# Kernel optimization log

Measured on AMD Instinct MI355X. Metric: run time of the kernel, lower is better.

## Reference

```python
import jax, jax.numpy as jnp
import numpy as np

B, P, T = 128, 196, 20
VOCAB, ENC, EMB, DEC, ATTN = 10000, 2048, 512, 512, 512


def _linear_params(key, out_dim, in_dim):
    kw, kb = jax.random.split(key)
    s = 1.0 / np.sqrt(in_dim)
    W = jax.random.uniform(kw, (out_dim, in_dim), minval=-s, maxval=s, dtype=jnp.float32)
    b = jax.random.uniform(kb, (out_dim,), minval=-s, maxval=s, dtype=jnp.float32)
    return W, b


def setup_inputs() -> dict:
    key = jax.random.key(0)
    ks = jax.random.split(key, 12)
    enc_w, enc_b = _linear_params(ks[0], ATTN, ENC)
    dec_w, dec_b = _linear_params(ks[1], ATTN, DEC)
    full_w, full_b = _linear_params(ks[2], 1, ATTN)
    W_ih, b_ih = _linear_params(ks[3], 4 * DEC, EMB + ENC)
    W_hh, b_hh = _linear_params(ks[4], 4 * DEC, DEC)
    ih_w, ih_b = _linear_params(ks[5], DEC, ENC)
    ic_w, ic_b = _linear_params(ks[6], DEC, ENC)
    fc_w, fc_b = _linear_params(ks[7], VOCAB, DEC)
    return {
        "encoder_out": jax.random.normal(ks[8], (B, P, ENC), dtype=jnp.float32),
        "captions": jax.random.randint(ks[9], (B, T), 0, VOCAB, dtype=jnp.int32),
        "lengths": jax.random.randint(ks[10], (B,), 1, T + 1, dtype=jnp.int32),
        "embedding": jax.random.normal(ks[11], (VOCAB, EMB), dtype=jnp.float32),
        "enc_attn_w": enc_w, "enc_attn_b": enc_b,
        "dec_attn_w": dec_w, "dec_attn_b": dec_b,
        "full_attn_w": full_w, "full_attn_b": full_b,
        "W_ih": W_ih, "b_ih": b_ih, "W_hh": W_hh, "b_hh": b_hh,
        "init_h_w": ih_w, "init_h_b": ih_b,
        "init_c_w": ic_w, "init_c_b": ic_b,
        "fc_w": fc_w, "fc_b": fc_b,
    }


def reference(encoder_out, captions, lengths, embedding,
              enc_attn_w, enc_attn_b, dec_attn_w, dec_attn_b,
              full_attn_w, full_attn_b, W_ih, b_ih, W_hh, b_hh,
              init_h_w, init_h_b, init_c_w, init_c_b, fc_w, fc_b):
    # init hidden state from mean-pooled encoder features
    mean_enc = encoder_out.mean(axis=1)                      # [B, ENC]
    h = mean_enc @ init_h_w.T + init_h_b                      # [B, DEC]
    c = mean_enc @ init_c_w.T + init_c_b

    # loop-invariant encoder projection for additive attention
    attn_enc = jnp.einsum('bpe,ae->bpa', encoder_out, enc_attn_w) + enc_attn_b  # [B, P, ATTN]

    embs = embedding[captions]                                # [B, T, EMB]
    embs_t = jnp.swapaxes(embs, 0, 1)                         # [T, B, EMB]

    dec = h.shape[1]

    def step(carry, emb_t):
        h, c = carry
        # additive attention
        attn_dec = h @ dec_attn_w.T + dec_attn_b              # [B, ATTN]
        energy = jnp.einsum('bpa,a->bp', jax.nn.relu(attn_enc + attn_dec[:, None, :]), full_attn_w[0]) + full_attn_b[0]
        alpha = jax.nn.softmax(energy, axis=1)                # [B, P]
        context = jnp.einsum('bpe,bp->be', encoder_out, alpha)  # [B, ENC]
        # LSTMCell
        x = jnp.concatenate([emb_t, context], axis=1)
        gates = x @ W_ih.T + b_ih + h @ W_hh.T + b_hh          # [B, 4*DEC]
        i, f, g, o = jnp.split(gates, 4, axis=1)
        c_new = jax.nn.sigmoid(f) * c + jax.nn.sigmoid(i) * jnp.tanh(g)
        h_new = jax.nn.sigmoid(o) * jnp.tanh(c_new)
        preds = h_new @ fc_w.T + fc_b                          # [B, VOCAB] (dropout in eval mode = identity)
        return (h_new, c_new), (preds, alpha)

    (_, _), (outputs_t, alphas_t) = jax.lax.scan(step, (h, c), embs_t)
    outputs = jnp.swapaxes(outputs_t, 0, 1)                   # [B, T, VOCAB]
    alphas = jnp.swapaxes(alphas_t, 0, 1)                     # [B, T, P]
    return outputs, alphas
```

## Files before the change

### kernel.cpp

```cpp
#include <hip/hip_runtime.h>

constexpr int kB = 128, kP = 196, kT = 20;
constexpr int kVocab = 10000, kEnc = 2048, kEmb = 512, kDec = 512, kAttn = 512;

typedef __bf16 b16x8 __attribute__((ext_vector_type(8)));
typedef __bf16 b16x4 __attribute__((ext_vector_type(4)));
typedef float f32x4 __attribute__((ext_vector_type(4)));
typedef unsigned short u16x4 __attribute__((ext_vector_type(4)));

__device__ __forceinline__ unsigned short f2bf(float f) {
  unsigned int u = __float_as_uint(f);
  u += 0x7fffu + ((u >> 16) & 1u);
  return (unsigned short)(u >> 16);
}
__device__ __forceinline__ float bf2f(unsigned short h) {
  return __uint_as_float(((unsigned int)h) << 16);
}

__device__ __forceinline__ void async16(const void* g, void* l) {
  __builtin_amdgcn_global_load_lds(
      (const __attribute__((address_space(1))) unsigned int*)g,
      (__attribute__((address_space(3))) unsigned int*)l, 16, 0, 0);
}

template <int MODE>
__global__ __launch_bounds__(256) void gemm128(
    const unsigned short* __restrict__ A, const unsigned short* __restrict__ W,
    const float* __restrict__ bias, unsigned short* __restrict__ Cb,
    float* __restrict__ Cf, int K, int Nv) {
  __shared__ unsigned short sA[2][128 * 64];
  __shared__ unsigned short sB[2][128 * 64];
  const int tid = threadIdx.x;
  const int lane = tid & 63, wave = tid >> 6;
  const int wm = wave >> 1, wn = wave & 1;
  const int q = lane >> 4, l = lane & 15;
  const int nwg = gridDim.x * gridDim.y;
  const int orig = blockIdx.y * gridDim.x + blockIdx.x;
  const int qc = nwg >> 3, rc = nwg & 7;
  const int xcd = orig & 7, o8 = orig >> 3;
  const int wg = (xcd < rc ? xcd * (qc + 1) : rc * (qc + 1) + (xcd - rc) * qc) + o8;
  const int m0 = (wg / gridDim.x) * 128, n0 = (wg % gridDim.x) * 128;
  const int row0 = tid & 127, ch0 = tid >> 7;
  const long arow = (long)(m0 + row0) * K;
  const long brow = (long)(n0 + row0) * K;
  f32x4 acc[4][4] = {};

  auto stage = [&](int buf, int k0) {
#pragma unroll
    for (int cc = 0; cc < 4; cc++) {
      const int ch = ch0 + cc * 2;
      async16(A + arow + k0 + ch * 8, &sA[buf][(ch * 128 + row0) * 8]);
      async16(W + brow + k0 + ch * 8, &sB[buf][(ch * 128 + row0) * 8]);
    }
  };

  stage(0, 0);
  __syncthreads();
  int cur = 0;
  for (int k0 = 0; k0 < K; k0 += 64) {
    const bool last = (k0 + 64 >= K);
    if (!last) stage(cur ^ 1, k0 + 64);
    b16x8 af[2][4], bfr[2][4];
#pragma unroll
    for (int u = 0; u < 2; u++) {
      const int cb = u * 4 + q;
#pragma unroll
      for (int i = 0; i < 4; i++)
        af[u][i] = *(const b16x8*)&sA[cur][(cb * 128 + wm * 64 + 16 * i + l) * 8];
#pragma unroll
      for (int j = 0; j < 4; j++)
        bfr[u][j] = *(const b16x8*)&sB[cur][(cb * 128 + wn * 64 + 16 * j + l) * 8];
    }
#pragma unroll
    for (int u = 0; u < 2; u++)
#pragma unroll
      for (int i = 0; i < 4; i++)
#pragma unroll
        for (int j = 0; j < 4; j++)
          acc[i][j] = __builtin_amdgcn_mfma_f32_16x16x32_bf16(af[u][i], bfr[u][j], acc[i][j], 0, 0, 0);
    if (!last) {
      __syncthreads();
      cur ^= 1;
    }
  }

#pragma unroll
  for (int i = 0; i < 4; i++) {
    const int row = m0 + wm * 64 + 16 * i + q * 4;
#pragma unroll
    for (int j = 0; j < 4; j++) {
      const int col = n0 + wn * 64 + 16 * j + l;
      if (col >= Nv) continue;
      const float bv = bias[col];
#pragma unroll
      for (int r = 0; r < 4; r++) {
        const float v = acc[i][j][r] + bv;
        if (MODE == 0) {
          Cb[(long)(row + r) * kAttn + col] = f2bf(v);
        } else {
          const int rr = row + r;
          Cf[((long)(rr & 127) * kT + (rr >> 7)) * (long)kVocab + col] = v;
        }
      }
    }
  }
}

template <bool A_BF16, bool OUT_BF16>
__global__ __launch_bounds__(256) void gemm_bt(
    const void* __restrict__ A_, const unsigned short* __restrict__ W,
    const float* __restrict__ bias, float* __restrict__ C,
    unsigned short* __restrict__ Cb, int M, int N, int K, long ldc) {
  const int lane = threadIdx.x & 63;
  const int wave = threadIdx.x >> 6;
  const int wm = wave >> 1, wn = wave & 1;
  const int m0 = blockIdx.y * 64 + wm * 32;
  const int n0 = blockIdx.x * 64 + wn * 32;
  const int q = lane >> 4;
  const int l = lane & 15;
  f32x4 acc[2][2] = {};
  const unsigned short* Ab = (const unsigned short*)A_;
  const float* Af = (const float*)A_;

  for (int k0 = 0; k0 < K; k0 += 32) {
    const int ka = k0 + q * 8;
    b16x8 af[2], wf[2];
#pragma unroll
    for (int i = 0; i < 2; i++) {
      int r = m0 + 16 * i + l;
      if (r >= M) r = M - 1;
      if (A_BF16) {
        af[i] = *(const b16x8*)(Ab + (long)r * K + ka);
      } else {
        const float* p = Af + (long)r * K + ka;
        const f32x4 lo = *(const f32x4*)p;
        const f32x4 hi = *(const f32x4*)(p + 4);
        b16x8 t;
#pragma unroll
        for (int j = 0; j < 4; j++) {
          ((unsigned short*)&t)[j] = f2bf(lo[j]);
          ((unsigned short*)&t)[4 + j] = f2bf(hi[j]);
        }
        af[i] = t;
      }
    }
#pragma unroll
    for (int j = 0; j < 2; j++) {
      int r = n0 + 16 * j + l;
      if (r >= N) r = N - 1;
      wf[j] = *(const b16x8*)(W + (long)r * K + ka);
    }
#pragma unroll
    for (int i = 0; i < 2; i++)
#pragma unroll
      for (int j = 0; j < 2; j++)
        acc[i][j] = __builtin_amdgcn_mfma_f32_16x16x32_bf16(af[i], wf[j], acc[i][j], 0, 0, 0);
  }

#pragma unroll
  for (int i = 0; i < 2; i++)
#pragma unroll
    for (int j = 0; j < 2; j++) {
      const int col = n0 + 16 * j + l;
      if (col >= N) continue;
      const float bv = bias ? bias[col] : 0.0f;
#pragma unroll
      for (int r = 0; r < 4; r++) {
        const int row = m0 + 16 * i + q * 4 + r;
        if (row >= M) continue;
        const float v = acc[i][j][r] + bv;
        if (OUT_BF16) Cb[(long)row * ldc + col] = f2bf(v);
        else          C[(long)row * ldc + col] = v;
      }
    }
}

__global__ __launch_bounds__(256) void adfc_kernel(
    const unsigned short* __restrict__ h_bf,
    const unsigned short* __restrict__ daw, const float* __restrict__ dab,
    float* __restrict__ ad_out) {
  const int blk = blockIdx.x;
  const int n0 = (blk & 7) * 64, m0 = (blk >> 3) * 64;
  const int lane = threadIdx.x & 63, wave = threadIdx.x >> 6;
  const int wm = wave >> 1, wn = wave & 1;
  const int q = lane >> 4, l = lane & 15;
  const int mi = m0 + wm * 32, ni = n0 + wn * 32;
  f32x4 acc[2][2] = {};

  for (int k0 = 0; k0 < 512; k0 += 64) {
    b16x8 af[2][2], wf[2][2];
#pragma unroll
    for (int u = 0; u < 2; u++) {
      const int ka = k0 + u * 32 + q * 8;
#pragma unroll
      for (int i = 0; i < 2; i++)
        af[u][i] = *(const b16x8*)(h_bf + (long)(mi + 16 * i + l) * 512 + ka);
#pragma unroll
      for (int j = 0; j < 2; j++)
        wf[u][j] = *(const b16x8*)(daw + (long)(ni + 16 * j + l) * 512 + ka);
    }
#pragma unroll
    for (int u = 0; u < 2; u++)
#pragma unroll
      for (int i = 0; i < 2; i++)
#pragma unroll
        for (int j = 0; j < 2; j++)
          acc[i][j] = __builtin_amdgcn_mfma_f32_16x16x32_bf16(af[u][i], wf[u][j], acc[i][j], 0, 0, 0);
  }
#pragma unroll
  for (int i = 0; i < 2; i++)
#pragma unroll
    for (int j = 0; j < 2; j++) {
      const int col = ni + 16 * j + l;
      const float bv = dab[col];
#pragma unroll
      for (int r = 0; r < 4; r++) {
        const int row = mi + 16 * i + q * 4 + r;
        ad_out[(long)row * 512 + col] = acc[i][j][r] + bv;
      }
    }
}

template <bool SRC_BF16>
__global__ __launch_bounds__(256) void attn2(
    const void* __restrict__ enc_, const unsigned short* __restrict__ attn_enc_bf,
    const float* __restrict__ ad_g, const float* __restrict__ faw,
    const float* __restrict__ fab, float* __restrict__ alphas,
    unsigned short* __restrict__ ctx, int t) {
  const int b = blockIdx.x;
  const int half = blockIdx.y;
  const int tid = threadIdx.x;
  const int lane = tid & 63, wave = tid >> 6;
  __shared__ float ad_s[512];
  __shared__ float e_sm[kP];
  __shared__ float red[4];
  __shared__ float cred[128][8];

  ad_s[tid] = ad_g[b * kAttn + tid];
  ad_s[tid + 256] = ad_g[b * kAttn + tid + 256];
  __syncthreads();

  float ad8[8], w8[8];
  const int a0 = lane * 8;
#pragma unroll
  for (int j = 0; j < 8; j++) { ad8[j] = ad_s[a0 + j]; w8[j] = faw[a0 + j]; }
  const float fb0 = fab[0];
  {
    int p = wave;
#pragma unroll 1
    for (int it = 0; it < 12; it++, p += 16) {
      b16x8 rv[4];
#pragma unroll
      for (int u = 0; u < 4; u++)
        rv[u] = *(const b16x8*)(attn_enc_bf + ((long)(b * kP + p + 4 * u)) * kAttn + a0);
      float s4[4];
#pragma unroll
      for (int u = 0; u < 4; u++) {
        float s = 0.f;
#pragma unroll
        for (int j = 0; j < 8; j++)
          s += w8[j] * fmaxf(bf2f(((const unsigned short*)&rv[u])[j]) + ad8[j], 0.f);
        s4[u] = s;
      }
#pragma unroll
      for (int u = 0; u < 4; u++) {
        float s = s4[u];
#pragma unroll
        for (int off = 32; off > 0; off >>= 1) s += __shfl_down(s, off, 64);
        if (lane == 0) e_sm[p + 4 * u] = s + fb0;
      }
    }
    {
      const b16x8 rv = *(const b16x8*)(attn_enc_bf + ((long)(b * kP + p)) * kAttn + a0);
      float s = 0.f;
#pragma unroll
      for (int j = 0; j < 8; j++)
        s += w8[j] * fmaxf(bf2f(((const unsigned short*)&rv)[j]) + ad8[j], 0.f);
#pragma unroll
      for (int off = 32; off > 0; off >>= 1) s += __shfl_down(s, off, 64);
      if (lane == 0) e_sm[p] = s + fb0;
    }
  }
  __syncthreads();

  const float v = (tid < kP) ? e_sm[tid] : -3.0e38f;
  float m = v;
#pragma unroll
  for (int off = 32; off > 0; off >>= 1) m = fmaxf(m, __shfl_down(m, off, 64));
  if (lane == 0) red[wave] = m;
  __syncthreads();
  m = fmaxf(fmaxf(red[0], red[1]), fmaxf(red[2], red[3]));
  const float ex = (tid < kP) ? expf(v - m) : 0.f;
  float s = ex;
#pragma unroll
  for (int off = 32; off > 0; off >>= 1) s += __shfl_down(s, off, 64);
  if (lane == 0) red[wave] = s;
  __syncthreads();
  s = red[0] + red[1] + red[2] + red[3];
  __syncthreads();
  const float alpha = ex / s;
  if (tid < kP) {
    e_sm[tid] = alpha;
    if (half == 0) alphas[((long)b * kT + t) * kP + tid] = alpha;
  }
  __syncthreads();

  const int pg = tid >> 7, th = tid & 127;
  const int e = half * 1024 + th * 8;
  float a8[8] = {};
  if (SRC_BF16) {
    const unsigned short* base = (const unsigned short*)enc_ + (long)b * kP * kEnc + e;
    int p = pg * 98;
#pragma unroll 1
    for (int it = 0; it < 12; it++, p += 8) {
      b16x8 rv[8];
#pragma unroll
      for (int u = 0; u < 8; u++) rv[u] = *(const b16x8*)(base + (long)(p + u) * kEnc);
#pragma unroll
      for (int u = 0; u < 8; u++) {
        const float a = e_sm[p + u];
#pragma unroll
        for (int j = 0; j < 8; j++) a8[j] += a * bf2f(((const unsigned short*)&rv[u])[j]);
      }
    }
#pragma unroll
    for (int u = 0; u < 2; u++, p++) {
      const float a = e_sm[p];
      const b16x8 rv = *(const b16x8*)(base + (long)p * kEnc);
#pragma unroll
      for (int j = 0; j < 8; j++) a8[j] += a * bf2f(((const unsigned short*)&rv)[j]);
    }
  } else {
    const float* base = (const float*)enc_ + (long)b * kP * kEnc + e;
    const int pbeg = pg * 98;
#pragma unroll 2
    for (int p = pbeg; p < pbeg + 98; p++) {
      const float a = e_sm[p];
      const f32x4 lo = *(const f32x4*)(base + (long)p * kEnc);
      const f32x4 hi = *(const f32x4*)(base + (long)p * kEnc + 4);
#pragma unroll
      for (int j = 0; j < 4; j++) { a8[j] += a * lo[j]; a8[4 + j] += a * hi[j]; }
    }
  }
  if (pg == 1) {
#pragma unroll
    for (int j = 0; j < 8; j++) cred[th][j] = a8[j];
  }
  __syncthreads();
  if (pg == 0) {
    u16x4 o0, o1;
#pragma unroll
    for (int j = 0; j < 4; j++) {
      o0[j] = f2bf(a8[j] + cred[th][j]);
      o1[j] = f2bf(a8[4 + j] + cred[th][4 + j]);
    }
    *(u16x4*)(ctx + (long)b * kEnc + e) = o0;
    *(u16x4*)(ctx + (long)b * kEnc + e + 4) = o1;
  }
}

__global__ __launch_bounds__(256) void gemm_gates(
    const unsigned short* __restrict__ embs_t, const unsigned short* __restrict__ ctx,
    const unsigned short* __restrict__ hbf, const unsigned short* __restrict__ Wih,
    const unsigned short* __restrict__ Whh, float* __restrict__ gates_part) {
  const int lane = threadIdx.x & 63;
  const int wave = threadIdx.x >> 6;
  const int wm = wave >> 1, wn = wave & 1;
  const int m0 = blockIdx.y * 64 + wm * 32;
  const int n0 = blockIdx.x * 64 + wn * 32;
  const int z = blockIdx.z;
  const int q = lane >> 4;
  const int l = lane & 15;
  f32x4 acc[2][2] = {};
  float* gout = gates_part + (long)z * kB * 2048;

  const int kbeg = z * 768, kend = kbeg + 768;
  for (int k0 = kbeg; k0 < kend; k0 += 64) {
    b16x8 af[2][2], wf[2][2];
#pragma unroll
    for (int u = 0; u < 2; u++) {
      const int k = k0 + u * 32;
#pragma unroll
      for (int i = 0; i < 2; i++) {
        const int r = m0 + 16 * i + l;
        const unsigned short* p;
        if (k < 512)        p = embs_t + (long)r * kEmb + k;
        else if (k < 2560)  p = ctx + (long)r * kEnc + (k - 512);
        else                p = hbf + (long)r * kDec + (k - 2560);
        af[u][i] = *(const b16x8*)(p + q * 8);
      }
#pragma unroll
      for (int j = 0; j < 2; j++) {
        const int r = n0 + 16 * j + l;
        const unsigned short* p;
        if (k < 2560) p = Wih + (long)r * 2560 + k;
        else          p = Whh + (long)r * 512 + (k - 2560);
        wf[u][j] = *(const b16x8*)(p + q * 8);
      }
    }
#pragma unroll
    for (int u = 0; u < 2; u++)
#pragma unroll
      for (int i = 0; i < 2; i++)
#pragma unroll
        for (int j = 0; j < 2; j++)
          acc[i][j] = __builtin_amdgcn_mfma_f32_16x16x32_bf16(af[u][i], wf[u][j], acc[i][j], 0, 0, 0);
  }
#pragma unroll
  for (int i = 0; i < 2; i++)
#pragma unroll
    for (int j = 0; j < 2; j++) {
      const int col = n0 + 16 * j + l;
#pragma unroll
      for (int r = 0; r < 4; r++) {
        const int row = m0 + 16 * i + q * 4 + r;
        gout[(long)row * 2048 + col] = acc[i][j][r];
      }
    }
}

__global__ __launch_bounds__(256) void lstm_ad(
    const float* __restrict__ gp, const float* __restrict__ bsum,
    float* __restrict__ c, unsigned short* __restrict__ h_out,
    const unsigned short* __restrict__ daw, const float* __restrict__ dab,
    float* __restrict__ ad_out) {
  const int b = blockIdx.x;
  const int tid = threadIdx.x;
  __shared__ float h_s[512];

#pragma unroll
  for (int u = 0; u < 2; u++) {
    const int d = tid + u * 256;
    float g4[4];
#pragma unroll
    for (int g = 0; g < 4; g++) {
      const int col = g * 512 + d;
      float s = bsum[col];
#pragma unroll
      for (int z = 0; z < 4; z++) s += gp[(long)z * kB * 2048 + (long)b * 2048 + col];
      g4[g] = s;
    }
    const float si = 1.f / (1.f + expf(-g4[0]));
    const float sf = 1.f / (1.f + expf(-g4[1]));
    const float so = 1.f / (1.f + expf(-g4[3]));
    const long idx = (long)b * 512 + d;
    const float cn = sf * c[idx] + si * tanhf(g4[2]);
    const float hn = so * tanhf(cn);
    c[idx] = cn;
    const unsigned short hb = f2bf(hn);
    h_out[idx] = hb;
    h_s[d] = bf2f(hb);
  }
  __syncthreads();

#pragma unroll
  for (int u = 0; u < 2; u++) {
    const int r = tid + u * 256;
    const unsigned short* wr = daw + (long)r * 512;
    float s0 = 0.f, s1 = 0.f, s2 = 0.f, s3 = 0.f;
#pragma unroll 1
    for (int k = 0; k < 512; k += 32) {
      b16x8 wv[4];
#pragma unroll
      for (int v = 0; v < 4; v++) wv[v] = *(const b16x8*)(wr + k + v * 8);
#pragma unroll
      for (int j = 0; j < 8; j++) s0 += h_s[k + j]      * bf2f(((const unsigned short*)&wv[0])[j]);
#pragma unroll
      for (int j = 0; j < 8; j++) s1 += h_s[k + 8 + j]  * bf2f(((const unsigned short*)&wv[1])[j]);
#pragma unroll
      for (int j = 0; j < 8; j++) s2 += h_s[k + 16 + j] * bf2f(((const unsigned short*)&wv[2])[j]);
#pragma unroll
      for (int j = 0; j < 8; j++) s3 += h_s[k + 24 + j] * bf2f(((const unsigned short*)&wv[3])[j]);
    }
    ad_out[(long)b * 512 + r] = ((s0 + s1) + (s2 + s3)) + dab[r];
  }
}

__global__ __launch_bounds__(256) void mean_cvt(
    const float* __restrict__ enc, unsigned short* __restrict__ enc_bf,
    unsigned short* __restrict__ mean_bf) {
  const int b = blockIdx.x;
  const int e = blockIdx.y * 1024 + threadIdx.x * 4;
  const float* base = enc + (long)b * kP * kEnc + e;
  unsigned short* ob = enc_bf + (long)b * kP * kEnc + e;
  f32x4 acc = {};
  int p = 0;
#pragma unroll 1
  for (int it = 0; it < 49; it++, p += 4) {
    f32x4 v[4];
#pragma unroll
    for (int u = 0; u < 4; u++) v[u] = *(const f32x4*)(base + (long)(p + u) * kEnc);
#pragma unroll
    for (int u = 0; u < 4; u++) {
      u16x4 o;
#pragma unroll
      for (int j = 0; j < 4; j++) { acc[j] += v[u][j]; o[j] = f2bf(v[u][j]); }
      *(u16x4*)(ob + (long)(p + u) * kEnc) = o;
    }
  }
  u16x4 om;
#pragma unroll
  for (int j = 0; j < 4; j++) om[j] = f2bf(acc[j] * (1.0f / 196.0f));
  *(u16x4*)(mean_bf + (long)b * kEnc + e) = om;
}

template <bool SRC_BF16>
__global__ __launch_bounds__(256) void mean_kernel(
    const void* __restrict__ enc_, unsigned short* __restrict__ mean_bf) {
  const int b = blockIdx.x;
  const int e = threadIdx.x * 8;
  float acc[8] = {};
  if (SRC_BF16) {
    const unsigned short* base = (const unsigned short*)enc_ + (long)b * kP * kEnc + e;
    for (int p = 0; p < kP; p++) {
      const b16x8 v = *(const b16x8*)(base + (long)p * kEnc);
#pragma unroll
      for (int j = 0; j < 8; j++) acc[j] += bf2f(((const unsigned short*)&v)[j]);
    }
  } else {
    const float* base = (const float*)enc_ + (long)b * kP * kEnc + e;
    for (int p = 0; p < kP; p++) {
      const f32x4 lo = *(const f32x4*)(base + (long)p * kEnc);
      const f32x4 hi = *(const f32x4*)(base + (long)p * kEnc + 4);
#pragma unroll
      for (int j = 0; j < 4; j++) { acc[j] += lo[j]; acc[4 + j] += hi[j]; }
    }
  }
#pragma unroll
  for (int j = 0; j < 8; j++)
    mean_bf[(long)b * kEnc + e + j] = f2bf(acc[j] * (1.0f / 196.0f));
}

__global__ __launch_bounds__(256) void f32_to_bf16_vec(
    const float* __restrict__ src, unsigned short* __restrict__ dst, long n4) {
  for (long i = blockIdx.x * (long)blockDim.x + threadIdx.x; i < n4;
       i += (long)gridDim.x * blockDim.x) {
    const f32x4 v = *(const f32x4*)(src + i * 4);
    u16x4 o;
#pragma unroll
    for (int j = 0; j < 4; j++) o[j] = f2bf(v[j]);
    *(u16x4*)(dst + i * 4) = o;
  }
}

__global__ __launch_bounds__(256) void gather_emb(
    const float* __restrict__ embedding, const int* __restrict__ captions,
    unsigned short* __restrict__ embs) {
  const int r = blockIdx.x;
  const int t = r >> 7, b = r & 127;
  const int cap = captions[b * kT + t];
  const float* src = embedding + (long)cap * kEmb;
  unsigned short* dst = embs + (long)r * kEmb;
  for (int i = threadIdx.x; i < kEmb; i += 256) dst[i] = f2bf(src[i]);
}

__global__ void bias_sum_k(const float* __restrict__ b1, const float* __restrict__ b2,
                           float* __restrict__ o) {
  const int i = blockIdx.x * 256 + threadIdx.x;
  if (i < 2048) o[i] = b1[i] + b2[i];
}

extern "C" void kernel_launch(void* const* d_in, const int* in_sizes, int n_in,
                              void* d_out, int out_size, void* d_ws, size_t ws_size,
                              hipStream_t stream) {
  const float* enc = (const float*)d_in[0];
  const int* captions = (const int*)d_in[1];
  const float* embedding = (const float*)d_in[3];
  const float* eaw = (const float*)d_in[4];
  const float* eab = (const float*)d_in[5];
  const float* daw = (const float*)d_in[6];
  const float* dab = (const float*)d_in[7];
  const float* faw = (const float*)d_in[8];
  const float* fab = (const float*)d_in[9];
  const float* Wih = (const float*)d_in[10];
  const float* bih = (const float*)d_in[11];
  const float* Whh = (const float*)d_in[12];
  const float* bhh = (const float*)d_in[13];
  const float* ihw = (const float*)d_in[14];
  const float* ihb = (const float*)d_in[15];
  const float* icw = (const float*)d_in[16];
  const float* icb = (const float*)d_in[17];
  const float* fcw = (const float*)d_in[18];
  const float* fcb = (const float*)d_in[19];

  float* out = (float*)d_out;
  float* alphas = out + (long)kB * kT * kVocab;

  char* ws = (char*)d_ws;
  size_t off = 0;
  auto alloc = [&](size_t bytes) -> void* {
    void* p = ws + off;
    off = (off + bytes + 255) & ~(size_t)255;
    return p;
  };
  unsigned short* attn_enc_bf = (unsigned short*)alloc((size_t)kB * kP * kAttn * 2);
  unsigned short* Wih_bf = (unsigned short*)alloc((size_t)2048 * 2560 * 2);
  unsigned short* Whh_bf = (unsigned short*)alloc((size_t)2048 * 512 * 2);
  unsigned short* fcw_bf = (unsigned short*)alloc((size_t)kVocab * kDec * 2);
  unsigned short* eaw_bf = (unsigned short*)alloc((size_t)kAttn * kEnc * 2);
  unsigned short* daw_bf = (unsigned short*)alloc((size_t)kAttn * kDec * 2);
  unsigned short* ihw_bf = (unsigned short*)alloc((size_t)kDec * kEnc * 2);
  unsigned short* icw_bf = (unsigned short*)alloc((size_t)kDec * kEnc * 2);
  unsigned short* embs_bf = (unsigned short*)alloc((size_t)kT * kB * kEmb * 2);
  unsigned short* mean_bf = (unsigned short*)alloc((size_t)kB * kEnc * 2);
  float* c = (float*)alloc((size_t)kB * kDec * 4);
  unsigned short* h_hist = (unsigned short*)alloc((size_t)(kT + 1) * kB * kDec * 2);
  float* ad_buf = (float*)alloc((size_t)kB * kAttn * 4);
  unsigned short* ctx_bf = (unsigned short*)alloc((size_t)kB * kEnc * 2);
  float* gates_part = (float*)alloc((size_t)4 * kB * 2048 * 4);
  float* bsum = (float*)alloc((size_t)2048 * 4);
  unsigned short* enc_bf = (unsigned short*)alloc((size_t)kB * kP * kEnc * 2);
  const bool have_enc_bf = (off <= ws_size);

  auto cvt = [&](const float* s, unsigned short* d, long n) {
    const long n4 = n / 4;
    long g = (n4 + 255) / 256;
    if (g > 2048) g = 2048;
    f32_to_bf16_vec<<<dim3((unsigned)g), dim3(256), 0, stream>>>(s, d, n4);
  };

  cvt(eaw, eaw_bf, (long)kAttn * kEnc);
  cvt(daw, daw_bf, (long)kAttn * kDec);
  cvt(Wih, Wih_bf, (long)2048 * 2560);
  cvt(Whh, Whh_bf, (long)2048 * 512);
  cvt(fcw, fcw_bf, (long)kVocab * kDec);
  cvt(ihw, ihw_bf, (long)kDec * kEnc);
  cvt(icw, icw_bf, (long)kDec * kEnc);
  bias_sum_k<<<8, 256, 0, stream>>>(bih, bhh, bsum);
  gather_emb<<<kT * kB, 256, 0, stream>>>(embedding, captions, embs_bf);
  if (have_enc_bf)
    mean_cvt<<<dim3(kB, 2), 256, 0, stream>>>(enc, enc_bf, mean_bf);
  else
    mean_kernel<false><<<kB, 256, 0, stream>>>(enc, mean_bf);

  gemm_bt<true, true><<<dim3(kDec / 64, kB / 64), 256, 0, stream>>>(
      mean_bf, ihw_bf, ihb, (float*)nullptr, h_hist, kB, kDec, kEnc, kDec);
  gemm_bt<true, false><<<dim3(kDec / 64, kB / 64), 256, 0, stream>>>(
      mean_bf, icw_bf, icb, c, (unsigned short*)nullptr, kB, kDec, kEnc, kDec);

  if (have_enc_bf)
    gemm128<0><<<dim3(kAttn / 128, (kB * kP) / 128), 256, 0, stream>>>(
        enc_bf, eaw_bf, eab, attn_enc_bf, (float*)nullptr, kEnc, kAttn);
  else
    gemm_bt<false, true><<<dim3(kAttn / 64, (kB * kP) / 64), 256, 0, stream>>>(
        enc, eaw_bf, eab, (float*)nullptr, attn_enc_bf, kB * kP, kAttn, kEnc, kAttn);

  adfc_kernel<<<16, 256, 0, stream>>>(h_hist, daw_bf, dab, ad_buf);

  for (int t = 0; t < kT; t++) {
    const unsigned short* hcur = h_hist + (long)t * kB * kDec;

    if (have_enc_bf)
      attn2<true><<<dim3(kB, 2), 256, 0, stream>>>(
          enc_bf, attn_enc_bf, ad_buf, faw, fab, alphas, ctx_bf, t);
    else
      attn2<false><<<dim3(kB, 2), 256, 0, stream>>>(
          enc, attn_enc_bf, ad_buf, faw, fab, alphas, ctx_bf, t);

    gemm_gates<<<dim3(2048 / 64, kB / 64, 4), 256, 0, stream>>>(
        embs_bf + (long)t * kB * kEmb, ctx_bf, hcur, Wih_bf, Whh_bf, gates_part);

    lstm_ad<<<kB, 256, 0, stream>>>(
        gates_part, bsum, c, h_hist + (long)(t + 1) * kB * kDec, daw_bf, dab, ad_buf);
  }

  gemm128<1><<<dim3((kVocab + 127) / 128, kT * kB / 128), 256, 0, stream>>>(
      h_hist + (long)kB * kDec, fcw_bf, fcb, (unsigned short*)nullptr, out, kDec, kVocab);
}
```

Before: 2.125 ms.

## Pipeline GEMM K-loop with 32-wide tiles and register-prefetch gates GEMM

```diff
diff --git a/kernel.cpp b/kernel.cpp
--- a/kernel.cpp
+++ b/kernel.cpp
@@ -28,8 +28,8 @@
     const unsigned short* __restrict__ A, const unsigned short* __restrict__ W,
     const float* __restrict__ bias, unsigned short* __restrict__ Cb,
     float* __restrict__ Cf, int K, int Nv) {
-  __shared__ unsigned short sA[2][128 * 64];
-  __shared__ unsigned short sB[2][128 * 64];
+  __shared__ unsigned short sA[2][128 * 32];
+  __shared__ unsigned short sB[2][128 * 32];
   const int tid = threadIdx.x;
   const int lane = tid & 63, wave = tid >> 6;
   const int wm = wave >> 1, wn = wave & 1;
@@ -41,47 +41,51 @@
   const int wg = (xcd < rc ? xcd * (qc + 1) : rc * (qc + 1) + (xcd - rc) * qc) + o8;
   const int m0 = (wg / gridDim.x) * 128, n0 = (wg % gridDim.x) * 128;
   const int row0 = tid & 127, ch0 = tid >> 7;
-  const long arow = (long)(m0 + row0) * K;
-  const long brow = (long)(n0 + row0) * K;
+  const long arow = (long)(m0 + row0) * K + ch0 * 8;
+  const long brow = (long)(n0 + row0) * K + ch0 * 8;
   f32x4 acc[4][4] = {};
 
   auto stage = [&](int buf, int k0) {
-#pragma unroll
-    for (int cc = 0; cc < 4; cc++) {
-      const int ch = ch0 + cc * 2;
-      async16(A + arow + k0 + ch * 8, &sA[buf][(ch * 128 + row0) * 8]);
-      async16(W + brow + k0 + ch * 8, &sB[buf][(ch * 128 + row0) * 8]);
-    }
+    async16(A + arow + k0, &sA[buf][(ch0 * 128 + row0) * 8]);
+    async16(A + arow + k0 + 16, &sA[buf][((ch0 + 2) * 128 + row0) * 8]);
+    async16(W + brow + k0, &sB[buf][(ch0 * 128 + row0) * 8]);
+    async16(W + brow + k0 + 16, &sB[buf][((ch0 + 2) * 128 + row0) * 8]);
   };
 
+  const int nt = K >> 5;
   stage(0, 0);
-  __syncthreads();
-  int cur = 0;
-  for (int k0 = 0; k0 < K; k0 += 64) {
-    const bool last = (k0 + 64 >= K);
-    if (!last) stage(cur ^ 1, k0 + 64);
-    b16x8 af[2][4], bfr[2][4];
-#pragma unroll
-    for (int u = 0; u < 2; u++) {
-      const int cb = u * 4 + q;
-#pragma unroll
-      for (int i = 0; i < 4; i++)
-        af[u][i] = *(const b16x8*)&sA[cur][(cb * 128 + wm * 64 + 16 * i + l) * 8];
+  stage(1, 32);
+
+  for (int t = 0; t < nt; ++t) {
+    const int cur = t & 1;
+    if (t + 1 < nt) {
+      asm volatile("s_waitcnt vmcnt(4)" ::: "memory");
+    } else {
+      asm volatile("s_waitcnt vmcnt(0)" ::: "memory");
+    }
+    __builtin_amdgcn_sched_barrier(0);
+    __builtin_amdgcn_s_barrier();
+    __builtin_amdgcn_sched_barrier(0);
+
+    b16x8 af[4], bfr[4];
+#pragma unroll
+    for (int i = 0; i < 4; i++)
+      af[i] = *(const b16x8*)&sA[cur][(q * 128 + wm * 64 + 16 * i + l) * 8];
+#pragma unroll
+    for (int j = 0; j < 4; j++)
+      bfr[j] = *(const b16x8*)&sB[cur][(q * 128 + wn * 64 + 16 * j + l) * 8];
+    __builtin_amdgcn_s_setprio(1);
+#pragma unroll
+    for (int i = 0; i < 4; i++)
 #pragma unroll
       for (int j = 0; j < 4; j++)
-        bfr[u][j] = *(const b16x8*)&sB[cur][(cb * 128 + wn * 64 + 16 * j + l) * 8];
-    }
-#pragma unroll
-    for (int u = 0; u < 2; u++)
-#pragma unroll
-      for (int i = 0; i < 4; i++)
-#pragma unroll
-        for (int j = 0; j < 4; j++)
-          acc[i][j] = __builtin_amdgcn_mfma_f32_16x16x32_bf16(af[u][i], bfr[u][j], acc[i][j], 0, 0, 0);
-    if (!last) {
-      __syncthreads();
-      cur ^= 1;
-    }
+        acc[i][j] = __builtin_amdgcn_mfma_f32_16x16x32_bf16(af[i], bfr[j], acc[i][j], 0, 0, 0);
+    __builtin_amdgcn_s_setprio(0);
+
+    __builtin_amdgcn_sched_barrier(0);
+    __builtin_amdgcn_s_barrier();
+    __builtin_amdgcn_sched_barrier(0);
+    if (t + 2 < nt) stage(cur, (t + 2) * 32);
   }
 
 #pragma unroll
@@ -359,6 +363,31 @@
   }
 }
 
+#define GATES_LOADK(pp, kk)                                                          \
+  {                                                                                  \
+    _Pragma("unroll")                                                                \
+    for (int u = 0; u < 2; u++) {                                                    \
+      const int k = (kk) + u * 32;                                                   \
+      _Pragma("unroll")                                                              \
+      for (int i = 0; i < 2; i++) {                                                  \
+        const int r = m0 + 16 * i + l;                                               \
+        const unsigned short* p;                                                     \
+        if (k < 512)        p = embs_t + (long)r * kEmb + k;                         \
+        else if (k < 2560)  p = ctx + (long)r * kEnc + (k - 512);                    \
+        else                p = hbf + (long)r * kDec + (k - 2560);                   \
+        af[pp][u][i] = *(const b16x8*)(p + q * 8);                                   \
+      }                                                                              \
+      _Pragma("unroll")                                                              \
+      for (int j = 0; j < 2; j++) {                                                  \
+        const int r = n0 + 16 * j + l;                                               \
+        const unsigned short* p;                                                     \
+        if (k < 2560) p = Wih + (long)r * 2560 + k;                                  \
+        else          p = Whh + (long)r * 512 + (k - 2560);                          \
+        wf[pp][u][j] = *(const b16x8*)(p + q * 8);                                   \
+      }                                                                              \
+    }                                                                                \
+  }
+
 __global__ __launch_bounds__(256) void gemm_gates(
     const unsigned short* __restrict__ embs_t, const unsigned short* __restrict__ ctx,
     const unsigned short* __restrict__ hbf, const unsigned short* __restrict__ Wih,
@@ -374,37 +403,20 @@
   f32x4 acc[2][2] = {};
   float* gout = gates_part + (long)z * kB * 2048;
 
-  const int kbeg = z * 768, kend = kbeg + 768;
-  for (int k0 = kbeg; k0 < kend; k0 += 64) {
-    b16x8 af[2][2], wf[2][2];
-#pragma unroll
-    for (int u = 0; u < 2; u++) {
-      const int k = k0 + u * 32;
-#pragma unroll
-      for (int i = 0; i < 2; i++) {
-        const int r = m0 + 16 * i + l;
-        const unsigned short* p;
-        if (k < 512)        p = embs_t + (long)r * kEmb + k;
-        else if (k < 2560)  p = ctx + (long)r * kEnc + (k - 512);
-        else                p = hbf + (long)r * kDec + (k - 2560);
-        af[u][i] = *(const b16x8*)(p + q * 8);
-      }
-#pragma unroll
-      for (int j = 0; j < 2; j++) {
-        const int r = n0 + 16 * j + l;
-        const unsigned short* p;
-        if (k < 2560) p = Wih + (long)r * 2560 + k;
-        else          p = Whh + (long)r * 512 + (k - 2560);
-        wf[u][j] = *(const b16x8*)(p + q * 8);
-      }
-    }
+  const int kbeg = z * 768;
+  b16x8 af[2][2][2], wf[2][2][2];
+  GATES_LOADK(0, kbeg);
+#pragma unroll 2
+  for (int kt = 0; kt < 12; kt++) {
+    const int pp = kt & 1;
+    if (kt < 11) GATES_LOADK(pp ^ 1, kbeg + (kt + 1) * 64);
 #pragma unroll
     for (int u = 0; u < 2; u++)
 #pragma unroll
       for (int i = 0; i < 2; i++)
 #pragma unroll
         for (int j = 0; j < 2; j++)
-          acc[i][j] = __builtin_amdgcn_mfma_f32_16x16x32_bf16(af[u][i], wf[u][j], acc[i][j], 0, 0, 0);
+          acc[i][j] = __builtin_amdgcn_mfma_f32_16x16x32_bf16(af[pp][u][i], wf[pp][u][j], acc[i][j], 0, 0, 0);
   }
 #pragma unroll
   for (int i = 0; i < 2; i++)
```

Result: faster. 2.052 ms (-3.4%).
